# Optimization experiments

Hardware: AMD Instinct MI355X
Metric: run time of the kernel (lower is better)

The kernel has to match this reference:

```python
import jax, jax.numpy as jnp
import numpy as np

N_NODE = 40000
DIM = 128
N_REL = 8
N_EDGES = 640000
HOP = 2
BS = 128
SQLEN = 50
STDV = 1.0 / np.sqrt(DIM)
LEAKY_SLOPE = 0.2


def setup_inputs() -> dict:
    key = jax.random.key(0)
    ks = jax.random.split(key, 12)
    inputs = jax.random.randint(ks[0], (BS, SQLEN), 0, N_NODE)
    A = jax.random.randint(ks[1], (BS, SQLEN, SQLEN), 0, 5)  # edge types 0..4
    mask_item = jnp.ones((BS, SQLEN), dtype=jnp.int32)
    embedding = jax.random.normal(ks[2], (N_NODE, DIM), jnp.float32) * STDV
    r_embed_w = jax.random.normal(ks[3], (N_REL, DIM), jnp.float32) * STDV
    trans_M = jax.random.normal(ks[4], (N_REL, DIM, DIM), jnp.float32) * STDV
    a_0 = jax.random.normal(ks[5], (DIM, 1), jnp.float32) * STDV
    a_1 = jax.random.normal(ks[6], (DIM, 1), jnp.float32) * STDV
    a_2 = jax.random.normal(ks[7], (DIM, 1), jnp.float32) * STDV
    a_3 = jax.random.normal(ks[8], (DIM, 1), jnp.float32) * STDV
    a_in_values = jax.random.uniform(ks[9], (N_EDGES,), jnp.float32)
    h_list = jax.random.randint(ks[10], (N_EDGES,), 0, N_NODE, dtype=jnp.int32)
    t_list = jax.random.randint(ks[11], (N_EDGES,), 0, N_NODE, dtype=jnp.int32)
    return {"inputs": inputs, "A": A, "mask_item": mask_item,
            "embedding": embedding, "r_embed_w": r_embed_w, "trans_M": trans_M,
            "a_0": a_0, "a_1": a_1, "a_2": a_2, "a_3": a_3,
            "a_in_values": a_in_values, "h_list": h_list, "t_list": t_list}


def local_agg(h, adj, a_stack):
    # h: (B,N,D); adj: (B,N,N) int codes; a_stack: (4,D)
    pair = h[:, :, None, :] * h[:, None, :, :]            # (B,N,N,D) pairwise product
    pair = jnp.where(pair > 0, pair, LEAKY_SLOPE * pair)  # LeakyReLU
    e = jnp.einsum('bijd,kd->bijk', pair, a_stack)        # 4 attention logits per pair
    alpha = jnp.full(e.shape[:-1], -9e15, e.dtype)
    for k in range(4):
        alpha = jnp.where(adj == k + 1, e[..., k], alpha)
    alpha = jax.nn.softmax(alpha, axis=-1)
    return jnp.einsum('bij,bjd->bid', alpha, h)


def spmm(v, rows, cols, x):
    # (sparse A) @ x with COO (rows, cols, v)
    return jax.ops.segment_sum(v[:, None] * x[cols], rows, num_segments=x.shape[0])


def sparse_row_softmax(v, rows, n):
    m = jax.ops.segment_max(v, rows, num_segments=n)
    e = jnp.exp(v - m[rows])
    s = jax.ops.segment_sum(e, rows, num_segments=n)
    return e / s[rows]


def update_attention(ego, h_list, t_list, trans_M, r_emb):
    # edges are block-sorted by relation with equal counts per relation
    per = h_list.shape[0] // N_REL
    vals = []
    for r in range(N_REL):
        sl = slice(r * per, (r + 1) * per)
        W = trans_M[r]                      # (D,D) TransR projection
        r_mul_h = ego[h_list[sl]] @ W
        r_mul_t = ego[t_list[sl]] @ W
        vals.append(jnp.sum(jnp.tanh(r_mul_t) * r_mul_h + r_emb[r], axis=1))
    return jnp.concatenate(vals)


def forward_fn(embedding, r_embed_w, trans_M, a_0, a_1, a_2, a_3,
               a_in_values, inputs, A, h_list, t_list):
    origin = embedding
    ego = embedding
    v = a_in_values
    all_embed = []
    for k in range(HOP):
        ego = spmm(v, h_list, t_list, ego)  # Aggregator (dropout in eval = identity)
        all_embed.append(ego)
        if k < HOP - 1:
            v_new = update_attention(ego, h_list, t_list, trans_M, r_embed_w)
            # torch assigns via .data with requires_grad=False -> constant
            v = jax.lax.stop_gradient(sparse_row_softmax(v_new, h_list, N_NODE))
    kg = sum(all_embed) / HOP
    a_stack = jnp.concatenate([a_0, a_1, a_2, a_3], axis=1).T  # (4,D)
    node_embeds = origin[inputs]            # (B,N,D)
    hidden = local_agg(node_embeds, A, a_stack)
    kg_embeds = kg[inputs]
    hidden = hidden + local_agg(kg_embeds, A, a_stack)
    return hidden, node_embeds


def reference(inputs, A, mask_item, embedding, r_embed_w, trans_M,
              a_0, a_1, a_2, a_3, a_in_values, h_list, t_list):
    return forward_fn(embedding, r_embed_w, trans_M, a_0, a_1, a_2, a_3,
                      a_in_values, inputs, A, h_list, t_list)
```

## Files before the change

kernel.cpp:

```cpp
#include <hip/hip_runtime.h>

#define N_NODE  40000
#define DIM     128
#define N_REL   8
#define N_EDGES 640000
#define PER_REL (N_EDGES / N_REL)
#define BS      128
#define SQ      50
#define NB      ((N_NODE + 255) / 256)
#define RSPLIT  8
#define RPB     (N_REL / RSPLIT)
#define CONVB   ((N_NODE * 64) / 256)
#define HISTB   (N_EDGES / 1024)

typedef unsigned int        u32;
typedef unsigned short      u16;
typedef unsigned char       u8;
typedef unsigned long long  u64;
typedef short  bf16x8 __attribute__((ext_vector_type(8)));
typedef float  f32x4  __attribute__((ext_vector_type(4)));
typedef float  f32x2  __attribute__((ext_vector_type(2)));
typedef u32    u32x4  __attribute__((ext_vector_type(4)));

#if __has_builtin(__builtin_amdgcn_cvt_pk_f32_fp8)
#define HW_FP8_DEC 1
#endif
#if __has_builtin(__builtin_amdgcn_cvt_pk_fp8_f32)
#define HW_FP8_ENC 1
#endif

__device__ __forceinline__ u16 f2bf(float f) {
  union { float f; u32 i; } c; c.f = f;
  u32 b = c.i;
  b += 0x7FFFu + ((b >> 16) & 1u);
  return (u16)(b >> 16);
}
__device__ __forceinline__ float bf2f(u32 u) {
  union { u32 i; float f; } c; c.i = u << 16; return c.f;
}
__device__ __forceinline__ float bflo(u32 w) {
  union { u32 i; float f; } c; c.i = w << 16; return c.f;
}
__device__ __forceinline__ float bfhi(u32 w) {
  union { u32 i; float f; } c; c.i = w & 0xffff0000u; return c.f;
}
__device__ __forceinline__ u32 pk2(float a, float b) {
  return (u32)f2bf(a) | ((u32)f2bf(b) << 16);
}
__device__ __forceinline__ float tanh_fast(float x) {
  float e = __expf(2.f * x);
  return 1.f - 2.f * __builtin_amdgcn_rcpf(e + 1.f);
}

__device__ __forceinline__ u32 f2fp8(float f) {
  union { float f; u32 i; } c; c.f = f;
  u32 b = c.i;
  u32 s = (b >> 24) & 0x80u;
  u32 mag = b & 0x7fffffffu;
  mag += 0x7FFFFu + ((mag >> 20) & 1u);
  int e8 = (int)(mag >> 23) - 120;
  if (e8 >= 16) return s | 0x7Eu;
  if (e8 <= 0) {
    float af = fabsf(f) * 512.f + 0.5f;
    int m2 = (int)af;
    if (m2 > 7) return s | 0x08u;
    return s | (u32)m2;
  }
  return s | ((u32)e8 << 3) | ((mag >> 20) & 7u);
}
__device__ __forceinline__ float fp8d(u32 byte) {
  u32 em = byte & 0x7fu;
  u32 e  = em >> 3;
  u32 M  = e ? (em & 7u) + 8u : em;
  u32 E  = e ? e : 1u;
  union { u32 i; float f; } sc; sc.i = (E + 117u) << 23;
  float v = (float)M * sc.f;
  return (byte & 0x80u) ? -v : v;
}
__device__ __forceinline__ float fp8dot4(u32 ta, u32 ha) {
#ifdef HW_FP8_DEC
  f32x2 t0 = __builtin_amdgcn_cvt_pk_f32_fp8(ta, 0);
  f32x2 t1 = __builtin_amdgcn_cvt_pk_f32_fp8(ta, 1);
  f32x2 h0 = __builtin_amdgcn_cvt_pk_f32_fp8(ha, 0);
  f32x2 h1 = __builtin_amdgcn_cvt_pk_f32_fp8(ha, 1);
  return t0.x * h0.x + t0.y * h0.y + t1.x * h1.x + t1.y * h1.y;
#else
  return fp8d(ta & 255u) * fp8d(ha & 255u)
       + fp8d((ta >> 8) & 255u) * fp8d((ha >> 8) & 255u)
       + fp8d((ta >> 16) & 255u) * fp8d((ha >> 16) & 255u)
       + fp8d(ta >> 24) * fp8d(ha >> 24);
#endif
}
__device__ __forceinline__ f32x2 fp8pair(u32 w) {
#ifdef HW_FP8_DEC
  return __builtin_amdgcn_cvt_pk_f32_fp8(w, 0);
#else
  f32x2 r; r.x = fp8d(w & 255u); r.y = fp8d((w >> 8) & 255u); return r;
#endif
}
__device__ __forceinline__ u16 fp8enc2(float a, float b) {
#ifdef HW_FP8_ENC
  u32 pk = (u32)__builtin_amdgcn_cvt_pk_fp8_f32(a, b, 0, 0);
  return (u16)(pk & 0xffffu);
#else
  return (u16)(f2fp8(a) | (f2fp8(b) << 8));
#endif
}

__global__ void __launch_bounds__(256)
prep_kernel(const float* __restrict__ emb, u32* __restrict__ embb,
            const float* __restrict__ W, u16* __restrict__ Wtb,
            const float* __restrict__ rembw, float* __restrict__ rsum8,
            const int* __restrict__ hl, int* __restrict__ cnt,
            int* __restrict__ rank) {
  int bid = blockIdx.x;
  if (bid < CONVB) {
    int i = bid * 256 + threadIdx.x;
    float2 v = reinterpret_cast<const float2*>(emb)[i];
    embb[i] = pk2(v.x, v.y);
  } else if (bid < CONVB + HISTB) {
    int base = (bid - CONVB) * 1024 + threadIdx.x;
    int hn[4], rk[4];
    #pragma unroll
    for (int j = 0; j < 4; j++) hn[j] = hl[base + j * 256];
    #pragma unroll
    for (int j = 0; j < 4; j++) rk[j] = atomicAdd(&cnt[hn[j]], 1);
    #pragma unroll
    for (int j = 0; j < 4; j++) rank[base + j * 256] = rk[j];
  } else if (bid < CONVB + HISTB + N_REL) {
    int r = bid - CONVB - HISTB;
    const float* Wr = W + (size_t)r * DIM * DIM;
    u16* o = Wtb + (size_t)r * DIM * DIM;
    for (int x = threadIdx.x; x < DIM * DIM; x += 256) {
      int n = x >> 7, k = x & 127;
      o[x] = f2bf(Wr[k * DIM + n]);
    }
  } else {
    int wv = threadIdx.x >> 6, lane = threadIdx.x & 63;
    for (int r = wv; r < N_REL; r += 4) {
      float s = rembw[r * DIM + lane] + rembw[r * DIM + 64 + lane];
      #pragma unroll
      for (int o = 32; o; o >>= 1) s += __shfl_xor(s, o, 64);
      if (lane == 0) rsum8[r] = s;
    }
  }
}

__global__ void bsum_kernel(const int* __restrict__ cnt, int* __restrict__ bsum) {
  __shared__ int sd[256];
  int i = blockIdx.x * 256 + threadIdx.x;
  sd[threadIdx.x] = (i < N_NODE) ? cnt[i] : 0;
  __syncthreads();
  for (int o = 128; o; o >>= 1) {
    if (threadIdx.x < o) sd[threadIdx.x] += sd[threadIdx.x + o];
    __syncthreads();
  }
  if (!threadIdx.x) bsum[blockIdx.x] = sd[0];
}

__global__ void scan_bsum_kernel(int* __restrict__ bsum) {
  __shared__ int sd[256];
  int t = threadIdx.x;
  int orig = (t < NB) ? bsum[t] : 0;
  sd[t] = orig;
  __syncthreads();
  for (int o = 1; o < 256; o <<= 1) {
    int v = (t >= o) ? sd[t - o] : 0;
    __syncthreads();
    sd[t] += v;
    __syncthreads();
  }
  if (t < NB) bsum[t] = sd[t] - orig;
}

__global__ void scan_final_kernel(const int* __restrict__ cnt, const int* __restrict__ bsum,
                                  int* __restrict__ rowptr) {
  __shared__ int sd[256];
  int t = threadIdx.x;
  int i = blockIdx.x * 256 + t;
  int orig = (i < N_NODE) ? cnt[i] : 0;
  sd[t] = orig;
  __syncthreads();
  for (int o = 1; o < 256; o <<= 1) {
    int v = (t >= o) ? sd[t - o] : 0;
    __syncthreads();
    sd[t] += v;
    __syncthreads();
  }
  int ex = sd[t] - orig + bsum[blockIdx.x];
  if (i < N_NODE) {
    rowptr[i] = ex;
    if (i == N_NODE - 1) rowptr[N_NODE] = ex + orig;
  }
}

__global__ void __launch_bounds__(256)
scatter_kernel(const int* __restrict__ hl, const int* __restrict__ tl,
               const float* __restrict__ ain, const int* __restrict__ rowptr,
               const int* __restrict__ rank, u64* __restrict__ pay64) {
  int base = blockIdx.x * 1024 + threadIdx.x;
  int pos[4];
  u64 pl[4];
  #pragma unroll
  for (int j = 0; j < 4; j++) {
    int e = base + j * 256;
    int hn = hl[e];
    pos[j] = rowptr[hn] + rank[e];
    int r = e / PER_REL;
    u32 lo = (u32)tl[e] | ((u32)hn << 16);
    u32 hi = (u32)r | ((u32)f2bf(ain[e]) << 16);
    pl[j] = ((u64)hi << 32) | lo;
  }
  #pragma unroll
  for (int j = 0; j < 4; j++) pay64[pos[j]] = pl[j];
}

__global__ void __launch_bounds__(256)
spmm_pay0(const u32* __restrict__ xb, const u64* __restrict__ pay64,
          const int* __restrict__ rowptr, u32* __restrict__ outb,
          u16* __restrict__ outf8) {
  int row = (blockIdx.x * 256 + threadIdx.x) >> 6;
  if (row >= N_NODE) return;
  int lane = threadIdx.x & 63;
  int lo = rowptr[row], n = rowptr[row + 1] - lo;
  float ax = 0.f, ay = 0.f;
  const u32* xl = xb + lane;
  int p = 0;
  for (; p + 7 < n; p += 8) {
    u64 q[8]; u32 w[8];
    #pragma unroll
    for (int j = 0; j < 8; j++) q[j] = pay64[lo + p + j];
    #pragma unroll
    for (int j = 0; j < 8; j++) w[j] = xl[(size_t)((u32)q[j] & 0xffffu) << 6];
    #pragma unroll
    for (int j = 0; j < 8; j++) {
      float v = bf2f((u32)(q[j] >> 48));
      ax += v * bflo(w[j]);
      ay += v * bfhi(w[j]);
    }
  }
  for (; p < n; p++) {
    u64 q0 = pay64[lo + p];
    float v0 = bf2f((u32)(q0 >> 48));
    u32 w0 = xl[(size_t)((u32)q0 & 0xffffu) << 6];
    ax += v0 * bflo(w0);
    ay += v0 * bfhi(w0);
  }
  outb[((size_t)row << 6) + lane] = pk2(ax, ay);
  outf8[((size_t)row << 6) + lane] = fp8enc2(ax, ay);
}

__global__ void __launch_bounds__(256)
score_spmm(const u8* __restrict__ projf8, const u16* __restrict__ xf8,
           const u64* __restrict__ pay64, const int* __restrict__ rowptr,
           const float* __restrict__ rsum8, float* __restrict__ vals,
           u32* __restrict__ outb) {
  int row = (blockIdx.x * 256 + threadIdx.x) >> 6;
  if (row >= N_NODE) return;
  int lane = threadIdx.x & 63;
  int g8 = lane >> 3, le8 = lane & 7;
  int lo = rowptr[row], n = rowptr[row + 1] - lo;

  float gsum = 0.f;
  for (int p0 = 0; p0 < n; p0 += 8) {
    int p = p0 + g8;
    bool valid = p < n;
    int t = 0, r = 0;
    if (valid) {
      u64 q = pay64[lo + p];
      t = (int)((u32)q & 0xffffu);
      r = (int)((u32)(q >> 32) & 0xffu);
    }
    float s = 0.f;
    if (valid) {
      const u8* base = projf8 + (size_t)r * N_NODE * 256;
      u32x4 tv = *reinterpret_cast<const u32x4*>(base + (size_t)t * 256 + le8 * 16);
      u32x4 hv = *reinterpret_cast<const u32x4*>(base + (size_t)row * 256 + 128 + le8 * 16);
      s = fp8dot4(tv[0], hv[0]) + fp8dot4(tv[1], hv[1])
        + fp8dot4(tv[2], hv[2]) + fp8dot4(tv[3], hv[3]);
    }
    #pragma unroll
    for (int o = 4; o; o >>= 1) s += __shfl_xor(s, o, 64);
    if (valid && le8 == 0) {
      float e = __expf(s + rsum8[r]);
      vals[lo + p] = e;
      gsum += e;
    }
  }
  float rs = (le8 == 0) ? gsum : 0.f;
  #pragma unroll
  for (int o = 32; o; o >>= 1) rs += __shfl_xor(rs, o, 64);
  float inv = (rs > 0.f) ? 1.f / rs : 0.f;

  float ax = 0.f, ay = 0.f;
  const u16* xl = xf8 + lane;
  int p = 0;
  for (; p + 7 < n; p += 8) {
    u32 w[8]; float v[8];
    #pragma unroll
    for (int j = 0; j < 8; j++) v[j] = vals[lo + p + j];
    #pragma unroll
    for (int j = 0; j < 8; j++)
      w[j] = xl[(size_t)((u32)pay64[lo + p + j] & 0xffffu) << 6];
    #pragma unroll
    for (int j = 0; j < 8; j++) {
      f32x2 xv = fp8pair(w[j]);
      ax += v[j] * xv.x;
      ay += v[j] * xv.y;
    }
  }
  for (; p < n; p++) {
    float v0 = vals[lo + p];
    u32 w0 = xl[(size_t)((u32)pay64[lo + p] & 0xffffu) << 6];
    f32x2 xv = fp8pair(w0);
    ax += v0 * xv.x;
    ay += v0 * xv.y;
  }
  outb[((size_t)row << 6) + lane] = pk2(ax * inv, ay * inv);
}

__global__ void __launch_bounds__(256)
proj_mfma4(const u32* __restrict__ egob, const u16* __restrict__ Wtb,
           u8* __restrict__ projf8) {
  __shared__ u16 Buf[128 * 136];
  int tid = threadIdx.x;
  int rel0  = (blockIdx.x & (RSPLIT - 1)) * RPB;
  int gbase = (blockIdx.x / RSPLIT) * 128;

  for (int x = tid; x < 128 * 64; x += 256) {
    int m = x >> 6, d2 = x & 63;
    int gm = gbase + m; if (gm >= N_NODE) gm = N_NODE - 1;
    u32 v = egob[((size_t)gm << 6) + d2];
    int byte = (m * 256 + d2 * 4) ^ ((m & 7) << 4);
    *reinterpret_cast<u32*>(reinterpret_cast<char*>(Buf) + byte) = v;
  }
  __syncthreads();

  int w = tid >> 6, lane = tid & 63;
  int l15 = lane & 15, g = lane >> 4;

  bf16x8 afr[2][4];
  #pragma unroll
  for (int kk = 0; kk < 4; kk++) {
    int kb = (kk * 32 + g * 8) * 2;
    #pragma unroll
    for (int mt = 0; mt < 2; mt++) {
      int m = w * 32 + mt * 16 + l15;
      int byte = (m * 256 + kb) ^ ((m & 7) << 4);
      afr[mt][kk] = *reinterpret_cast<bf16x8*>(reinterpret_cast<char*>(Buf) + byte);
    }
  }
  __syncthreads();

  for (int rr = 0; rr < RPB; rr++) {
    int r = rel0 + rr;
    const u32* Wr32 = reinterpret_cast<const u32*>(Wtb + (size_t)r * DIM * DIM);
    for (int x = tid; x < 128 * 64; x += 256) {
      int n = x >> 6, k2 = x & 63;
      int byte = (n * 256 + k2 * 4) ^ ((n & 7) << 4);
      *reinterpret_cast<u32*>(reinterpret_cast<char*>(Buf) + byte) = Wr32[x];
    }
    __syncthreads();

    f32x4 acc[2][8];
    #pragma unroll
    for (int mt = 0; mt < 2; mt++)
      #pragma unroll
      for (int nt = 0; nt < 8; nt++) acc[mt][nt] = (f32x4){0.f, 0.f, 0.f, 0.f};

    #pragma unroll
    for (int kk = 0; kk < 4; kk++) {
      int kb = (kk * 32 + g * 8) * 2;
      #pragma unroll
      for (int nt = 0; nt < 8; nt++) {
        int n = nt * 16 + l15;
        int byte = (n * 256 + kb) ^ ((n & 7) << 4);
        bf16x8 b = *reinterpret_cast<bf16x8*>(reinterpret_cast<char*>(Buf) + byte);
        acc[0][nt] = __builtin_amdgcn_mfma_f32_16x16x32_bf16(afr[0][kk], b, acc[0][nt], 0, 0, 0);
        acc[1][nt] = __builtin_amdgcn_mfma_f32_16x16x32_bf16(afr[1][kk], b, acc[1][nt], 0, 0, 0);
      }
    }
    __syncthreads();

    char* BufB = reinterpret_cast<char*>(Buf);
    #pragma unroll
    for (int mt = 0; mt < 2; mt++)
      #pragma unroll
      for (int reg = 0; reg < 4; reg++) {
        int row = w * 32 + mt * 16 + g * 4 + reg;
        char* rb = BufB + row * 272;
        #pragma unroll
        for (int nt = 0; nt < 8; nt++) {
          float v = acc[mt][nt][reg];
          int col = nt * 16 + l15;
#ifdef HW_FP8_ENC
          u32 pk = (u32)__builtin_amdgcn_cvt_pk_fp8_f32(tanh_fast(v), v, 0, 0);
          rb[col]       = (char)(pk & 255u);
          rb[128 + col] = (char)((pk >> 8) & 255u);
#else
          rb[col]       = (char)f2fp8(tanh_fast(v));
          rb[128 + col] = (char)f2fp8(v);
#endif
        }
      }
    __syncthreads();

    const u32x4* Cs = reinterpret_cast<const u32x4*>(Buf);
    u32* dst = reinterpret_cast<u32*>(projf8 + (size_t)r * N_NODE * 256);
    for (int x = tid; x < 128 * 16; x += 256) {
      int row = x >> 4, q = x & 15;
      int node = gbase + row;
      if (node < N_NODE) {
        u32x4 v = Cs[row * 17 + q];
        *reinterpret_cast<u32x4*>(dst + ((size_t)node << 6) + q * 4) = v;
      }
    }
    __syncthreads();
  }
}

__global__ void __launch_bounds__(512)
local_agg4(const float* __restrict__ emb, const u32* __restrict__ ego1b,
           const u32* __restrict__ ego2b, const int* __restrict__ inp,
           const int* __restrict__ Aadj,
           const float* __restrict__ a0, const float* __restrict__ a1,
           const float* __restrict__ a2, const float* __restrict__ a3,
           float* __restrict__ out_hidden, float* __restrict__ out_node,
           float* __restrict__ tmpK) {
  __shared__ u16   Qb[64 * 256];
  __shared__ u16   hTb[128 * 64];
  __shared__ float aC[4][256];
  __shared__ float S[4][64 * 66];
  __shared__ u16   P[64 * 64];
  __shared__ float sinv[64];
  __shared__ int   adjL[SQ * SQ];

  int b = blockIdx.x >> 1, which = blockIdx.x & 1;
  int tid = threadIdx.x;

  {
    int k = tid >> 7, d = tid & 127;
    const float* ap = (k == 0) ? a0 : (k == 1) ? a1 : (k == 2) ? a2 : a3;
    float av = ap[d];
    aC[k][d] = 0.6f * av;
    aC[k][128 + d] = 0.4f * av;
  }
  for (int x = tid; x < SQ * SQ; x += 512) adjL[x] = Aadj[b * SQ * SQ + x];
  for (int x = tid; x < 128 * 16; x += 512) {
    int d = x >> 4, j = 48 + (x & 15);
    if (j >= 50) {
      int byte = (d * 128 + j * 2) ^ ((d & 7) << 4);
      *reinterpret_cast<u16*>(reinterpret_cast<char*>(hTb) + byte) = 0;
    }
  }
  for (int x = tid; x < SQ * 64; x += 512) {
    int j = x >> 6, d2 = (x & 63) << 1;
    int node = inp[b * SQ + j];
    float v0, v1;
    if (which == 0) {
      float2 vv = *reinterpret_cast<const float2*>(emb + (size_t)node * DIM + d2);
      v0 = vv.x; v1 = vv.y;
      *reinterpret_cast<float2*>(out_node + (size_t)(b * SQ + j) * DIM + d2) = vv;
    } else {
      u32 w1 = ego1b[((size_t)node << 6) + (d2 >> 1)];
      u32 w2 = ego2b[((size_t)node << 6) + (d2 >> 1)];
      v0 = 0.5f * (bf2f(w1 & 0xffffu) + bf2f(w2 & 0xffffu));
      v1 = 0.5f * (bf2f(w1 >> 16) + bf2f(w2 >> 16));
    }
    u16 b0 = f2bf(v0), b1 = f2bf(v1);
    { int byte = (j * 512 + d2 * 2) ^ ((j & 7) << 4);
      *reinterpret_cast<u32*>(reinterpret_cast<char*>(Qb) + byte) = (u32)b0 | ((u32)b1 << 16); }
    { int byte = (j * 512 + 256 + d2 * 2) ^ ((j & 7) << 4);
      u32 m0 = b0 & 0x7fffu, m1 = b1 & 0x7fffu;
      *reinterpret_cast<u32*>(reinterpret_cast<char*>(Qb) + byte) = m0 | (m1 << 16); }
    { int byte = (d2 * 128 + j * 2) ^ ((d2 & 7) << 4);
      *reinterpret_cast<u16*>(reinterpret_cast<char*>(hTb) + byte) = b0; }
    { int byte = ((d2 + 1) * 128 + j * 2) ^ (((d2 + 1) & 7) << 4);
      *reinterpret_cast<u16*>(reinterpret_cast<char*>(hTb) + byte) = b1; }
  }
  __syncthreads();

  int w = tid >> 6, lane = tid & 63;
  int l15 = lane & 15, g = lane >> 4;

  {
    int k = w >> 1, half = w & 1;
    const float* aCk = aC[k];
    f32x4 acc[2][4];
    #pragma unroll
    for (int mt = 0; mt < 2; mt++)
      #pragma unroll
      for (int nt = 0; nt < 4; nt++) acc[mt][nt] = (f32x4){0.f, 0.f, 0.f, 0.f};
    for (int ks = 0; ks < 8; ks++) {
      int kb = ks * 32 + g * 8;
      float4 c01 = *reinterpret_cast<const float4*>(aCk + kb);
      float4 c23 = *reinterpret_cast<const float4*>(aCk + kb + 4);
      bf16x8 afr[2];
      #pragma unroll
      for (int mt = 0; mt < 2; mt++) {
        int m = (half * 2 + mt) * 16 + l15;
        int byte = (m * 512 + kb * 2) ^ ((m & 7) << 4);
        union { bf16x8 v; u32 u[4]; } qv, o;
        qv.v = *reinterpret_cast<bf16x8*>(reinterpret_cast<char*>(Qb) + byte);
        o.u[0] = pk2(bf2f(qv.u[0] & 0xffffu) * c01.x, bf2f(qv.u[0] >> 16) * c01.y);
        o.u[1] = pk2(bf2f(qv.u[1] & 0xffffu) * c01.z, bf2f(qv.u[1] >> 16) * c01.w);
        o.u[2] = pk2(bf2f(qv.u[2] & 0xffffu) * c23.x, bf2f(qv.u[2] >> 16) * c23.y);
        o.u[3] = pk2(bf2f(qv.u[3] & 0xffffu) * c23.z, bf2f(qv.u[3] >> 16) * c23.w);
        afr[mt] = o.v;
      }
      #pragma unroll
      for (int nt = 0; nt < 4; nt++) {
        int n = nt * 16 + l15;
        int byte = (n * 512 + kb * 2) ^ ((n & 7) << 4);
        bf16x8 bfr = *reinterpret_cast<bf16x8*>(reinterpret_cast<char*>(Qb) + byte);
        acc[0][nt] = __builtin_amdgcn_mfma_f32_16x16x32_bf16(afr[0], bfr, acc[0][nt], 0, 0, 0);
        acc[1][nt] = __builtin_amdgcn_mfma_f32_16x16x32_bf16(afr[1], bfr, acc[1][nt], 0, 0, 0);
      }
    }
    #pragma unroll
    for (int mt = 0; mt < 2; mt++)
      #pragma unroll
      for (int nt = 0; nt < 4; nt++)
        #pragma unroll
        for (int reg = 0; reg < 4; reg++) {
          int m = (half * 2 + mt) * 16 + g * 4 + reg;
          int n = nt * 16 + l15;
          S[k][m * 66 + n] = acc[mt][nt][reg];
        }
  }
  __syncthreads();

  for (int i = w; i < SQ; i += 8) {
    float p = 0.f;
    if (lane < SQ) {
      int sel = adjL[i * SQ + lane];
      if (sel > 0) p = __expf(S[sel - 1][i * 66 + lane]);
    }
    float s = p;
    #pragma unroll
    for (int off = 32; off; off >>= 1) s += __shfl_xor(s, off, 64);
    if (lane == 0) sinv[i] = (s > 0.f) ? 1.f / s : 0.f;
    int byte = (i * 128 + lane * 2) ^ ((i & 7) << 4);
    *reinterpret_cast<u16*>(reinterpret_cast<char*>(P) + byte) = f2bf(p);
  }
  __syncthreads();

  {
    int mt = w >> 1, ng = w & 1;
    f32x4 acc[4];
    #pragma unroll
    for (int nt = 0; nt < 4; nt++) acc[nt] = (f32x4){0.f, 0.f, 0.f, 0.f};
    #pragma unroll
    for (int ks = 0; ks < 2; ks++) {
      int kb = ks * 32 + g * 8;
      int m = mt * 16 + l15;
      int abyte = (m * 128 + kb * 2) ^ ((m & 7) << 4);
      bf16x8 afr = *reinterpret_cast<bf16x8*>(reinterpret_cast<char*>(P) + abyte);
      #pragma unroll
      for (int nt = 0; nt < 4; nt++) {
        int d = (ng * 4 + nt) * 16 + l15;
        int byte = (d * 128 + kb * 2) ^ ((d & 7) << 4);
        bf16x8 bfr = *reinterpret_cast<bf16x8*>(reinterpret_cast<char*>(hTb) + byte);
        acc[nt] = __builtin_amdgcn_mfma_f32_16x16x32_bf16(afr, bfr, acc[nt], 0, 0, 0);
      }
    }
    float* dst = which ? tmpK : out_hidden;
    #pragma unroll
    for (int nt = 0; nt < 4; nt++)
      #pragma unroll
      for (int reg = 0; reg < 4; reg++) {
        int i = mt * 16 + g * 4 + reg;
        if (i < SQ) {
          int d = (ng * 4 + nt) * 16 + l15;
          dst[(size_t)(b * SQ + i) * DIM + d] = acc[nt][reg] * sinv[i];
        }
      }
  }
}

__global__ void add_kernel(float* __restrict__ out, const float* __restrict__ add) {
  int i = blockIdx.x * 256 + threadIdx.x;
  float4 a = reinterpret_cast<const float4*>(add)[i];
  float4 o = reinterpret_cast<float4*>(out)[i];
  o.x += a.x; o.y += a.y; o.z += a.z; o.w += a.w;
  reinterpret_cast<float4*>(out)[i] = o;
}

extern "C" void kernel_launch(void* const* d_in, const int* in_sizes, int n_in,
                              void* d_out, int out_size, void* d_ws, size_t ws_size,
                              hipStream_t stream) {
  const int*   inputs = (const int*)d_in[0];
  const int*   Aadj   = (const int*)d_in[1];
  const float* emb    = (const float*)d_in[3];
  const float* rembw  = (const float*)d_in[4];
  const float* transM = (const float*)d_in[5];
  const float* a0     = (const float*)d_in[6];
  const float* a1     = (const float*)d_in[7];
  const float* a2     = (const float*)d_in[8];
  const float* a3     = (const float*)d_in[9];
  const float* ain    = (const float*)d_in[10];
  const int*   hl     = (const int*)d_in[11];
  const int*   tl     = (const int*)d_in[12];

  u32*   ego1b    = (u32*)d_ws;
  u32*   ego2b    = ego1b + (size_t)N_NODE * 64;
  u32*   embb     = ego2b + (size_t)N_NODE * 64;
  u8*    projf8   = (u8*)(embb + (size_t)N_NODE * 64);
  u16*   Wtb      = (u16*)(projf8 + (size_t)N_REL * N_NODE * 256);
  u64*   pay64    = (u64*)(Wtb + (size_t)N_REL * DIM * DIM);
  float* vals     = (float*)(pay64 + N_EDGES);
  int*   rank     = (int*)(vals + N_EDGES);
  int*   cnt      = rank + N_EDGES;
  int*   rowptr   = cnt + N_NODE;
  int*   bsum     = rowptr + N_NODE + 64;
  float* rsum8    = (float*)(bsum + 256);
  float* tmpK     = rsum8 + 64;
  u16*   ego1f8   = (u16*)(tmpK + (size_t)BS * SQ * DIM);

  float* out_hidden = (float*)d_out;
  float* out_node   = out_hidden + (size_t)BS * SQ * DIM;

  hipMemsetAsync(cnt, 0, N_NODE * sizeof(int), stream);
  prep_kernel<<<CONVB + HISTB + N_REL + 1, 256, 0, stream>>>(
      emb, embb, transM, Wtb, rembw, rsum8, hl, cnt, rank);
  bsum_kernel<<<NB, 256, 0, stream>>>(cnt, bsum);
  scan_bsum_kernel<<<1, 256, 0, stream>>>(bsum);
  scan_final_kernel<<<NB, 256, 0, stream>>>(cnt, bsum, rowptr);
  scatter_kernel<<<N_EDGES / 1024, 256, 0, stream>>>(hl, tl, ain, rowptr, rank, pay64);

  spmm_pay0<<<(N_NODE * 64) / 256, 256, 0, stream>>>(embb, pay64, rowptr, ego1b, ego1f8);

  proj_mfma4<<<((N_NODE + 127) / 128) * RSPLIT, 256, 0, stream>>>(ego1b, Wtb, projf8);

  score_spmm<<<(N_NODE * 64) / 256, 256, 0, stream>>>(projf8, ego1f8, pay64, rowptr,
                                                      rsum8, vals, ego2b);

  local_agg4<<<BS * 2, 512, 0, stream>>>(emb, ego1b, ego2b, inputs, Aadj,
                                         a0, a1, a2, a3, out_hidden, out_node, tmpK);
  add_kernel<<<(BS * SQ * DIM / 4) / 256, 256, 0, stream>>>(out_hidden, tmpK);
}
```

Before: 213.5 us.

## Fuse score and aggregation in score_spmm into single pass over edges

The score_spmm kernel used to compute edge scores, write exp values to a global vals buffer, and then make a second pass that re-read vals and the neighbor indices to aggregate fp8 features. Now each 8-lane group gathers the neighbor's 16 fp8 feature bytes in the same pass and accumulates e*x into 16 per-lane registers. A cross-group shuffle reduction then combines partial sums before one group writes the normalized row. This removes the vals round-trip and the second index/gather pass, at the cost of more registers and 48 extra shuffles per row.

```diff
diff --git a/kernel.cpp b/kernel.cpp
--- a/kernel.cpp
+++ b/kernel.cpp
@@ -253,70 +253,72 @@
 __global__ void __launch_bounds__(256)
 score_spmm(const u8* __restrict__ projf8, const u16* __restrict__ xf8,
            const u64* __restrict__ pay64, const int* __restrict__ rowptr,
-           const float* __restrict__ rsum8, float* __restrict__ vals,
-           u32* __restrict__ outb) {
+           const float* __restrict__ rsum8, u32* __restrict__ outb) {
   int row = (blockIdx.x * 256 + threadIdx.x) >> 6;
   if (row >= N_NODE) return;
   int lane = threadIdx.x & 63;
   int g8 = lane >> 3, le8 = lane & 7;
   int lo = rowptr[row], n = rowptr[row + 1] - lo;
-
+  const u8* xf8b = reinterpret_cast<const u8*>(xf8);
+
+  float acc[16];
+  #pragma unroll
+  for (int i = 0; i < 16; i++) acc[i] = 0.f;
   float gsum = 0.f;
+
   for (int p0 = 0; p0 < n; p0 += 8) {
     int p = p0 + g8;
     bool valid = p < n;
-    int t = 0, r = 0;
+    int r = 0;
+    u32x4 xv = (u32x4){0u, 0u, 0u, 0u};
+    float s = 0.f;
     if (valid) {
       u64 q = pay64[lo + p];
-      t = (int)((u32)q & 0xffffu);
+      int t = (int)((u32)q & 0xffffu);
       r = (int)((u32)(q >> 32) & 0xffu);
-    }
-    float s = 0.f;
-    if (valid) {
       const u8* base = projf8 + (size_t)r * N_NODE * 256;
       u32x4 tv = *reinterpret_cast<const u32x4*>(base + (size_t)t * 256 + le8 * 16);
       u32x4 hv = *reinterpret_cast<const u32x4*>(base + (size_t)row * 256 + 128 + le8 * 16);
+      xv = *reinterpret_cast<const u32x4*>(xf8b + (size_t)t * 128 + le8 * 16);
       s = fp8dot4(tv[0], hv[0]) + fp8dot4(tv[1], hv[1])
         + fp8dot4(tv[2], hv[2]) + fp8dot4(tv[3], hv[3]);
     }
     #pragma unroll
     for (int o = 4; o; o >>= 1) s += __shfl_xor(s, o, 64);
-    if (valid && le8 == 0) {
+    if (valid) {
       float e = __expf(s + rsum8[r]);
-      vals[lo + p] = e;
-      gsum += e;
-    }
-  }
-  float rs = (le8 == 0) ? gsum : 0.f;
+      if (le8 == 0) gsum += e;
+      #pragma unroll
+      for (int c = 0; c < 4; c++) {
+        f32x2 loP = fp8pair(xv[c]);
+        f32x2 hiP = fp8pair(xv[c] >> 16);
+        acc[c * 4 + 0] += e * loP.x;
+        acc[c * 4 + 1] += e * loP.y;
+        acc[c * 4 + 2] += e * hiP.x;
+        acc[c * 4 + 3] += e * hiP.y;
+      }
+    }
+  }
+
+  float rs = gsum;
   #pragma unroll
   for (int o = 32; o; o >>= 1) rs += __shfl_xor(rs, o, 64);
   float inv = (rs > 0.f) ? 1.f / rs : 0.f;
 
-  float ax = 0.f, ay = 0.f;
-  const u16* xl = xf8 + lane;
-  int p = 0;
-  for (; p + 7 < n; p += 8) {
-    u32 w[8]; float v[8];
-    #pragma unroll
-    for (int j = 0; j < 8; j++) v[j] = vals[lo + p + j];
-    #pragma unroll
-    for (int j = 0; j < 8; j++)
-      w[j] = xl[(size_t)((u32)pay64[lo + p + j] & 0xffffu) << 6];
-    #pragma unroll
-    for (int j = 0; j < 8; j++) {
-      f32x2 xv = fp8pair(w[j]);
-      ax += v[j] * xv.x;
-      ay += v[j] * xv.y;
-    }
-  }
-  for (; p < n; p++) {
-    float v0 = vals[lo + p];
-    u32 w0 = xl[(size_t)((u32)pay64[lo + p] & 0xffffu) << 6];
-    f32x2 xv = fp8pair(w0);
-    ax += v0 * xv.x;
-    ay += v0 * xv.y;
-  }
-  outb[((size_t)row << 6) + lane] = pk2(ax * inv, ay * inv);
+  #pragma unroll
+  for (int i = 0; i < 16; i++) {
+    #pragma unroll
+    for (int o = 8; o < 64; o <<= 1) acc[i] += __shfl_xor(acc[i], o, 64);
+  }
+
+  if (g8 == 0) {
+    u32 slot[8];
+    #pragma unroll
+    for (int j = 0; j < 8; j++) slot[j] = pk2(acc[2 * j] * inv, acc[2 * j + 1] * inv);
+    u32* dst = outb + ((size_t)row << 6) + le8 * 8;
+    *reinterpret_cast<u32x4*>(dst)     = (u32x4){slot[0], slot[1], slot[2], slot[3]};
+    *reinterpret_cast<u32x4*>(dst + 4) = (u32x4){slot[4], slot[5], slot[6], slot[7]};
+  }
 }
 
 __global__ void __launch_bounds__(256)
@@ -608,8 +610,7 @@
   u8*    projf8   = (u8*)(embb + (size_t)N_NODE * 64);
   u16*   Wtb      = (u16*)(projf8 + (size_t)N_REL * N_NODE * 256);
   u64*   pay64    = (u64*)(Wtb + (size_t)N_REL * DIM * DIM);
-  float* vals     = (float*)(pay64 + N_EDGES);
-  int*   rank     = (int*)(vals + N_EDGES);
+  int*   rank     = (int*)(pay64 + N_EDGES);
   int*   cnt      = rank + N_EDGES;
   int*   rowptr   = cnt + N_NODE;
   int*   bsum     = rowptr + N_NODE + 64;
@@ -633,7 +634,7 @@
   proj_mfma4<<<((N_NODE + 127) / 128) * RSPLIT, 256, 0, stream>>>(ego1b, Wtb, projf8);
 
   score_spmm<<<(N_NODE * 64) / 256, 256, 0, stream>>>(projf8, ego1f8, pay64, rowptr,
-                                                      rsum8, vals, ego2b);
+                                                      rsum8, ego2b);
 
   local_agg4<<<BS * 2, 512, 0, stream>>>(emb, ego1b, ego2b, inputs, Aadj,
                                          a0, a1, a2, a3, out_hidden, out_node, tmpK);
```

Measured after the change: 214.3 us. Within noise of the previous version (+0.3%).
